# Kernel optimization log

Measured on AMD Instinct MI355X. Metric: run time of the kernel, lower is better.

The kernel has to match this reference:

```python
import jax, jax.numpy as jnp
import numpy as np

B, C_IN, T, H, W = 8, 8, 12, 128, 128
HID = 32
K = 3


def _conv2d(x, w, b):
    # x: (B, Cin, H, W), w: (Cout, Cin, K, K) -> SAME padding, stride 1
    y = jax.lax.conv_general_dilated(
        x, w, window_strides=(1, 1), padding='SAME',
        dimension_numbers=('NCHW', 'OIHW', 'NCHW'))
    return y + b[None, :, None, None]


def setup_inputs() -> dict:
    key = jax.random.key(0)
    k1, k2, k3, k4, k5 = jax.random.split(key, 5)
    x = jax.random.normal(k1, (B, C_IN, T, H, W), dtype=jnp.float32)
    cin = C_IN + HID
    scale = 1.0 / np.sqrt(cin * K * K)
    W_gates = jax.random.normal(k2, (2 * HID, cin, K, K), dtype=jnp.float32) * scale
    b_gates = jax.random.normal(k3, (2 * HID,), dtype=jnp.float32) * 0.01
    W_can = jax.random.normal(k4, (HID, cin, K, K), dtype=jnp.float32) * scale
    b_can = jax.random.normal(k5, (HID,), dtype=jnp.float32) * 0.01
    return {"x": x, "W_gates": W_gates, "b_gates": b_gates,
            "W_can": W_can, "b_can": b_can}


def reference(x, W_gates, b_gates, W_can, b_can):
    # x: (B, C, T, H, W) -> swap to time-major for the recurrence
    xs = jnp.transpose(x, (2, 0, 1, 3, 4))  # (T, B, C, H, W)
    h0 = jnp.zeros((x.shape[0], HID, x.shape[3], x.shape[4]), dtype=x.dtype)

    def step(h, x_t):
        comb = jnp.concatenate([x_t, h], axis=1)          # (B, C+HID, H, W)
        gates = jax.nn.sigmoid(_conv2d(comb, W_gates, b_gates))
        reset, update = jnp.split(gates, 2, axis=1)       # each (B, HID, H, W)
        comb2 = jnp.concatenate([x_t, reset * h], axis=1)
        cand = jnp.tanh(_conv2d(comb2, W_can, b_can))
        h_next = (1.0 - update) * h + update * cand
        return h_next, h_next

    h_last, ys = jax.lax.scan(step, h0, xs)               # ys: (T, B, HID, H, W)
    out = jnp.transpose(ys, (1, 2, 0, 3, 4))              # (B, HID, T, H, W) — swap back
    return out, h_last
```

## Files before the change

### kernel.cpp

```cpp
#include <hip/hip_runtime.h>
#include <hip/hip_bf16.h>
#include <hip/hip_fp16.h>
#include <cmath>

#define BB   8
#define CIN  8
#define TT   12
#define HH   128
#define WW   128
#define HID  32
#define CCOMB 40
#define HW   (HH * WW)
#define NBLK 512

#define S1    44
#define T1W   20
#define OFF2  17600
#define S2    36
#define OFFU  29264
#define SMEM_U16 38480

typedef __attribute__((ext_vector_type(8))) short sv8;
typedef __attribute__((ext_vector_type(4))) short sv4;
typedef __attribute__((ext_vector_type(4))) float f32x4;
typedef unsigned short u16;
typedef unsigned long long ull;

__device__ inline u16 f2bf(float f) {
    union { float f; unsigned u; } v; v.f = f;
    unsigned u = v.u;
    return (u16)((u + 0x7FFFu + ((u >> 16) & 1u)) >> 16);
}
__device__ inline float bf2f(u16 h) {
    union { unsigned u; float f; } v; v.u = ((unsigned)h) << 16; return v.f;
}
__device__ inline float sigmoid_fast(float x) { return 1.f / (1.f + __expf(-x)); }
__device__ inline float tanh_fast(float z) {
    float a = fabsf(z);
    float r = 1.f - 2.f / (__expf(2.f * a) + 1.f);
    return copysignf(r, z);
}

__device__ __forceinline__ void band_rc(int i, int& r, int& c) {
    if (i < 40)      { r = i / 20;            c = i % 20; }
    else if (i < 80) { int j = i - 40; r = 18 + j / 20; c = j % 20; }
    else             { int j = i - 80; r = 2 + (j >> 2);
                       int k = j & 3;  c = (k < 2) ? k : 16 + k; }
}

__device__ inline sv8 gather_wfrag(const float* __restrict__ W,
                                   int co, int g, int kx, int ks) {
    int k0 = ks * 32 + g * 8;
    sv8 f;
    if (k0 < 120) {
        int ky  = k0 / 40;
        int ci0 = k0 - ky * 40;
#pragma unroll
        for (int i = 0; i < 8; ++i)
            f[i] = (short)f2bf(W[(((size_t)co * CCOMB + ci0 + i) * 3 + ky) * 3 + kx]);
    } else {
#pragma unroll
        for (int i = 0; i < 8; ++i) f[i] = 0;
    }
    return f;
}

__global__ void pack_weights(const float* __restrict__ Wg,
                             const float* __restrict__ Wc,
                             u16* __restrict__ pack) {
    int tid = blockIdx.x * blockDim.x + threadIdx.x;
    if (tid >= 6 * 12 * 64) return;
    int lane = tid & 63;
    int f    = (tid >> 6) % 12;
    int Gall = tid / (12 * 64);
    int kx = f >> 2, ks = f & 3;
    int g = lane >> 4;
    sv8 v;
    if (Gall < 4) v = gather_wfrag(Wg, Gall * 16 + (lane & 15), g, kx, ks);
    else          v = gather_wfrag(Wc, (Gall - 4) * 16 + (lane & 15), g, kx, ks);
    *(sv8*)&pack[(size_t)tid * 8] = v;
}

__global__ __launch_bounds__(256) void x_to_bf16(const float* __restrict__ x,
                                                 u16* __restrict__ xbf) {
    int gid = blockIdx.x * 256 + threadIdx.x;
    if (gid >= BB * TT * HW) return;
    int p  = gid & (HW - 1);
    int bt = gid >> 14;
    int t = bt % TT, b = bt / TT;
    sv8 v;
#pragma unroll
    for (int c = 0; c < 8; ++c)
        v[c] = (short)f2bf(x[(((size_t)b * CIN + c) * TT + t) * HW + p]);
    *(sv8*)&xbf[(size_t)gid * 8] = v;
}

#define MFMA16(A, B, C) __builtin_amdgcn_mfma_f32_16x16x32_bf16(A, B, C, 0, 0, 0)

#define GATES_TILE(YY, XX, LVAL, UVALQ)                                        \
    {                                                                          \
        int pb = ((YY) * T1W + (XX)) * S1;                                     \
        f32x4 aA = {0.f,0.f,0.f,0.f}, aB = {0.f,0.f,0.f,0.f};                  \
        _Pragma("unroll")                                                      \
        for (int kx = 0; kx < 3; ++kx)                                         \
        _Pragma("unroll")                                                      \
        for (int ks = 0; ks < 4; ++ks) {                                       \
            int a = pb + kx * S1 + koff1[ks];                                  \
            sv4 lo = *(const sv4*)&smem[a];                                    \
            sv4 hi = *(const sv4*)&smem[a + 4];                                \
            sv8 bv = __builtin_shufflevector(lo, hi, 0,1,2,3,4,5,6,7);         \
            aA = MFMA16(wfA[kx*4+ks], bv, aA);                                 \
            aB = MFMA16(wfB[kx*4+ks], bv, aB);                                 \
        }                                                                      \
        if (coPair == 0) {                                                     \
            int ctr = pb + 21 * S1 + 8;                                        \
            sv4 h4A = *(const sv4*)&smem[ctr + co0A];                          \
            sv4 h4B = *(const sv4*)&smem[ctr + co0B];                          \
            sv4 rhA, rhB;                                                      \
            _Pragma("unroll")                                                  \
            for (int r = 0; r < 4; ++r) {                                      \
                rhA[r] = (short)f2bf(sigmoid_fast(aA[r] + bgA[r]) * bf2f((u16)h4A[r])); \
                rhB[r] = (short)f2bf(sigmoid_fast(aB[r] + bgB[r]) * bf2f((u16)h4B[r])); \
            }                                                                  \
            if (LVAL) {                                                        \
                int o2 = OFF2 + ((YY) * 18 + (XX)) * S2;                       \
                *(sv4*)&smem[o2 + co0A] = rhA;                                 \
                *(sv4*)&smem[o2 + co0B] = rhB;                                 \
            }                                                                  \
        } else {                                                               \
            sv4 uA, uB;                                                        \
            _Pragma("unroll")                                                  \
            for (int r = 0; r < 4; ++r) {                                      \
                uA[r] = (short)__half_as_ushort(__float2half(sigmoid_fast(aA[r] + bgA[r]))); \
                uB[r] = (short)__half_as_ushort(__float2half(sigmoid_fast(aB[r] + bgB[r]))); \
            }                                                                  \
            if ((LVAL) && (UVALQ)) {                                           \
                int uo = OFFU + (((YY) - 1) * 16 + ((XX) - 1)) * S2;           \
                *(sv4*)&smem[uo + (co0A - 32)] = uA;                           \
                *(sv4*)&smem[uo + (co0B - 32)] = uB;                           \
            }                                                                  \
        }                                                                      \
    }

__global__ __launch_bounds__(256)
__attribute__((amdgpu_waves_per_eu(2, 2)))
void gru_persist(
    const u16* __restrict__ xbf, const u16* __restrict__ wpack,
    const float* __restrict__ bg, const float* __restrict__ bc,
    u16* __restrict__ hG, int* __restrict__ flags,
    float* __restrict__ out, float* __restrict__ hlast)
{
    __shared__ __align__(16) u16 smem[SMEM_U16];
    const int id = blockIdx.x;
    const int b = id & 7, tau = id >> 3;
    const int bx = tau & 7, by = tau >> 3;
    const int x0 = bx * 16, y0 = by * 16;
    const int tid = threadIdx.x, lane = tid & 63, w = tid >> 6;
    const int m = lane & 15, g = lane >> 4;

    int nbr = -1;
    if (tid < 8) {
        const int dxs[8] = {-1, 0, 1, -1, 1, -1, 0, 1};
        const int dys[8] = {-1, -1, -1, 0, 0, 1, 1, 1};
        int nx = bx + dxs[tid], ny = by + dys[tid];
        if ((unsigned)nx < 8u && (unsigned)ny < 8u)
            nbr = ((ny * 8 + nx) * 8 + b);
    }

    int koff1[4], coffC[4], kstrC[4];
    bool isX[4];
#pragma unroll
    for (int ks = 0; ks < 4; ++ks) {
        int k0 = ks * 32 + g * 8;
        int ky = 0, ci0 = 0;
        if (k0 < 120) { ky = k0 / 40; ci0 = k0 - ky * 40; }
        koff1[ks] = ky * (T1W * S1) + ci0;
        isX[ks]   = (ci0 == 0);
        coffC[ks] = isX[ks] ? ky * (T1W * S1) : ky * (18 * S2) + (ci0 - 8);
        kstrC[ks] = isX[ks] ? S1 : S2;
    }

    const int coPair = w >> 1;
    const int parity = w & 1;
    const int co0A = coPair * 32 + g * 4;
    const int co0B = co0A + 16;
    const int grpA = coPair * 2, grpB = grpA + 1;

    const int j0 = w * 4;
    int rowb1[4], rowb2[4];
#pragma unroll
    for (int jr = 0; jr < 4; ++jr) {
        rowb1[jr] = ((j0 + jr + 1) * T1W + m + 1) * S1;
        rowb2[jr] = OFF2 + ((j0 + jr) * 18 + m) * S2;
    }

    f32x4 bgA = *(const f32x4*)&bg[co0A];
    f32x4 bgB = *(const f32x4*)&bg[co0B];
    f32x4 bcA = *(const f32x4*)&bc[g * 4];
    f32x4 bcB = *(const f32x4*)&bc[16 + g * 4];
    const int cA = g * 4, cB = 16 + g * 4;

    for (int i = tid; i < 3200; i += 256) {
        int px = i >> 3, q = i & 7;
        *(ull*)&smem[px * S1 + 8 + q * 4] = 0ull;
    }

    const u16* xbB = xbf + (size_t)b * TT * HW * 8;
    const size_t planeElems = (size_t)BB * HW * 32;

    for (int t = 0; t < TT; ++t) {
        const u16* hGr = hG + (size_t)(t & 1) * planeElems + (size_t)b * HW * 32;
        u16*       hGw = hG + (size_t)((t + 1) & 1) * planeElems + (size_t)b * HW * 32;

        sv8 wfA[12], wfB[12];
#pragma unroll
        for (int f = 0; f < 12; ++f) {
            wfA[f] = *(const sv8*)&wpack[(((size_t)grpA * 12 + f) * 64 + lane) * 8];
            wfB[f] = *(const sv8*)&wpack[(((size_t)grpB * 12 + f) * 64 + lane) * 8];
        }

        const u16* xb = xbB + (size_t)t * HW * 8;
        for (int idx = tid; idx < 400; idx += 256) {
            int r = idx / 20, c = idx - r * 20;
            int gy = y0 + r - 2, gx = x0 + c - 2;
            sv8 v = {};
            if ((unsigned)gy < 128u && (unsigned)gx < 128u)
                v = *(const sv8*)&xb[(size_t)(gy * WW + gx) * 8];
            *(sv4*)&smem[idx * S1]     = __builtin_shufflevector(v, v, 0,1,2,3);
            *(sv4*)&smem[idx * S1 + 4] = __builtin_shufflevector(v, v, 4,5,6,7);
        }
        __syncthreads();

        for (int nt = parity; nt < 13; nt += 2) {
            int i = nt * 16 + m;
            bool lval = (i < 196);
            if (i > 195) i = 195;
            int q14 = i / 14;
            int yy = 2 + q14, xx = 2 + (i - q14 * 14);
            GATES_TILE(yy, xx, lval, true);
        }

        if (t > 0) {
            if (tid < 8 && nbr >= 0) {
                while (__hip_atomic_load(&flags[nbr * 32], __ATOMIC_RELAXED,
                                         __HIP_MEMORY_SCOPE_AGENT) < t)
                    __builtin_amdgcn_s_sleep(2);
            }
        }
        __syncthreads();

        for (int idx = tid; idx < 1152; idx += 256) {
            int i = idx >> 3, q = idx & 7;
            int r, c; band_rc(i, r, c);
            int gy = y0 + r - 2, gx = x0 + c - 2;
            ull v = 0;
            if ((unsigned)gy < 128u && (unsigned)gx < 128u)
                v = __hip_atomic_load((const ull*)&hGr[(size_t)(gy * WW + gx) * 32 + q * 4],
                                      __ATOMIC_RELAXED, __HIP_MEMORY_SCOPE_AGENT);
            *(ull*)&smem[(r * T1W + c) * S1 + 8 + q * 4] = v;
        }
        __syncthreads();

        for (int nt = parity; nt < 8; nt += 2) {
            int e = nt * 16 + m;
            int yy, xx;
            if (e < 36)       { int q = e / 18;        yy = q;       xx = e - q * 18; }
            else if (e < 72)  { int j = e - 36; int q = j / 18; yy = 16 + q; xx = j - q * 18; }
            else if (e < 100) { int j = e - 72;  yy = 2 + (j >> 1); xx = (j & 1); }
            else              { int j = e - 100; yy = 2 + (j >> 1); xx = 16 + (j & 1); }
            bool uval = (yy >= 1 && yy <= 16 && xx >= 1 && xx <= 16);
            GATES_TILE(yy, xx, true, uval);
        }

        sv8 wcA[12], wcB[12];
#pragma unroll
        for (int f = 0; f < 12; ++f) {
            wcA[f] = *(const sv8*)&wpack[(((size_t)4 * 12 + f) * 64 + lane) * 8];
            wcB[f] = *(const sv8*)&wpack[(((size_t)5 * 12 + f) * 64 + lane) * 8];
        }
        __syncthreads();

        f32x4 a2A[4], a2B[4];
#pragma unroll
        for (int jr = 0; jr < 4; ++jr) {
            a2A[jr] = (f32x4){0.f,0.f,0.f,0.f};
            a2B[jr] = (f32x4){0.f,0.f,0.f,0.f};
        }
#pragma unroll
        for (int kx = 0; kx < 3; ++kx)
#pragma unroll
            for (int ks = 0; ks < 4; ++ks) {
#pragma unroll
                for (int jr = 0; jr < 4; ++jr) {
                    int a = (isX[ks] ? rowb1[jr] : rowb2[jr]) + coffC[ks] + kx * kstrC[ks];
                    sv4 lo = *(const sv4*)&smem[a];
                    sv4 hi = *(const sv4*)&smem[a + 4];
                    sv8 bv = __builtin_shufflevector(lo, hi, 0,1,2,3,4,5,6,7);
                    a2A[jr] = MFMA16(wcA[kx*4+ks], bv, a2A[jr]);
                    a2B[jr] = MFMA16(wcB[kx*4+ks], bv, a2B[jr]);
                }
            }

#pragma unroll
        for (int jr = 0; jr < 4; ++jr) {
            int j = j0 + jr;
            int gy = y0 + j, gx = x0 + m;
            int ctr = ((j + 2) * T1W + m + 2) * S1 + 8;
            int ub  = OFFU + (j * 16 + m) * S2;
            sv4 h4A = *(const sv4*)&smem[ctr + cA];
            sv4 h4B = *(const sv4*)&smem[ctr + cB];
            sv4 u4A = *(const sv4*)&smem[ub + cA];
            sv4 u4B = *(const sv4*)&smem[ub + cB];
            sv4 hnA, hnB;
#pragma unroll
            for (int r = 0; r < 4; ++r) {
                float cv = tanh_fast(a2A[jr][r] + bcA[r]);
                float uu = __half2float(__ushort_as_half((u16)u4A[r]));
                float hn = (1.f - uu) * bf2f((u16)h4A[r]) + uu * cv;
                a2A[jr][r] = hn; hnA[r] = (short)f2bf(hn);
                cv = tanh_fast(a2B[jr][r] + bcB[r]);
                uu = __half2float(__ushort_as_half((u16)u4B[r]));
                hn = (1.f - uu) * bf2f((u16)h4B[r]) + uu * cv;
                a2B[jr][r] = hn; hnB[r] = (short)f2bf(hn);
            }
            *(sv4*)&smem[ctr + cA] = hnA;
            *(sv4*)&smem[ctr + cB] = hnB;
            if (j <= 1 || j >= 14 || m <= 1 || m >= 14) {
                union { sv4 s; ull u; } ca, cb; ca.s = hnA; cb.s = hnB;
                ull* base = (ull*)&hGw[(size_t)(gy * WW + gx) * 32];
                __hip_atomic_store(base + (cA >> 2), ca.u, __ATOMIC_RELAXED,
                                   __HIP_MEMORY_SCOPE_AGENT);
                __hip_atomic_store(base + (cB >> 2), cb.u, __ATOMIC_RELAXED,
                                   __HIP_MEMORY_SCOPE_AGENT);
            }
        }

        asm volatile("s_waitcnt vmcnt(0)" ::: "memory");
        __syncthreads();
        if (tid == 0)
            __hip_atomic_store(&flags[id * 32], t + 1, __ATOMIC_RELAXED,
                               __HIP_MEMORY_SCOPE_AGENT);

#pragma unroll
        for (int jr = 0; jr < 4; ++jr) {
            int j = j0 + jr;
            int gy = y0 + j, gx = x0 + m;
#pragma unroll
            for (int r = 0; r < 4; ++r) {
                __builtin_nontemporal_store(a2A[jr][r],
                    &out[(((size_t)b * HID + cA + r) * TT + t) * HW + (size_t)gy * WW + gx]);
                __builtin_nontemporal_store(a2B[jr][r],
                    &out[(((size_t)b * HID + cB + r) * TT + t) * HW + (size_t)gy * WW + gx]);
                if (t == TT - 1) {
                    __builtin_nontemporal_store(a2A[jr][r],
                        &hlast[((size_t)b * HID + cA + r) * HW + (size_t)gy * WW + gx]);
                    __builtin_nontemporal_store(a2B[jr][r],
                        &hlast[((size_t)b * HID + cB + r) * HW + (size_t)gy * WW + gx]);
                }
            }
        }
    }
}

extern "C" void kernel_launch(void* const* d_in, const int* in_sizes, int n_in,
                              void* d_out, int out_size, void* d_ws, size_t ws_size,
                              hipStream_t stream) {
    const float* x  = (const float*)d_in[0];
    const float* Wg = (const float*)d_in[1];
    const float* bg = (const float*)d_in[2];
    const float* Wc = (const float*)d_in[3];
    const float* bc = (const float*)d_in[4];

    float* out   = (float*)d_out;
    float* hlast = out + (size_t)BB * HID * TT * HW;

    const size_t PLANEB = (size_t)BB * HW * 32 * sizeof(u16);
    const size_t PACKB  = (size_t)6 * 12 * 64 * 8 * sizeof(u16);
    const size_t FLAGB  = (size_t)NBLK * 32 * sizeof(int);
    char* ws = (char*)d_ws;
    u16* hG    = (u16*)ws;
    u16* wpack = (u16*)(ws + 2 * PLANEB);
    int* flags = (int*)(ws + 2 * PLANEB + PACKB);
    u16* xbf   = (u16*)(ws + 2 * PLANEB + PACKB + FLAGB);

    pack_weights<<<(6 * 12 * 64 + 255) / 256, 256, 0, stream>>>(Wg, Wc, wpack);
    x_to_bf16<<<(BB * TT * HW) / 256, 256, 0, stream>>>(x, xbf);
    hipMemsetAsync(hG, 0, PLANEB, stream);
    hipMemsetAsync(flags, 0, FLAGB, stream);

    gru_persist<<<NBLK, 256, 0, stream>>>(xbf, wpack, bg, bc, hG, flags,
                                          out, hlast);
}
```

Measured before the change: 471.7 us.

## Exchange halo through per-block compact outbox with 16-byte coherent loads/stores

Replaces the full-size global hidden-state planes with a compact per-block outbox holding only the 144 border pixels each block's neighbours need. The halo is now written from LDS after a barrier as 16-byte coherent stores and read as 16-byte loads with precomputed offsets, instead of 8-byte atomic accesses scattered across the image. Candidate-weight loading is moved earlier so it overlaps the halo fetch. The change adds an extra barrier and inline asm with sc0/sc1 cache bits, and relies on the outbox mapping being correct for neighbours at tile edges.

Measured after the change: 561.5 us. 1.19x slower.

```diff
diff --git a/kernel.cpp b/kernel.cpp
--- a/kernel.cpp
+++ b/kernel.cpp
@@ -20,9 +20,13 @@
 #define OFFU  29264
 #define SMEM_U16 38480
 
+#define OB_BLK   4608
+#define OB_PLANE ((size_t)NBLK * OB_BLK)
+
 typedef __attribute__((ext_vector_type(8))) short sv8;
 typedef __attribute__((ext_vector_type(4))) short sv4;
 typedef __attribute__((ext_vector_type(4))) float f32x4;
+typedef __attribute__((ext_vector_type(4))) unsigned u32x4;
 typedef unsigned short u16;
 typedef unsigned long long ull;
 
@@ -47,6 +51,29 @@
     else             { int j = i - 80; r = 2 + (j >> 2);
                        int k = j & 3;  c = (k < 2) ? k : 16 + k; }
 }
+
+__device__ __forceinline__ void obox_rc(int px, int& r, int& c) {
+    if (px < 32)       { r = px >> 4;               c = px & 15; }
+    else if (px < 64)  { int i = px - 32;  r = 14 + (i >> 4); c = i & 15; }
+    else if (px < 96)  { int i = px - 64;  r = i >> 1;        c = i & 1; }
+    else if (px < 128) { int i = px - 96;  r = i >> 1;        c = 14 + (i & 1); }
+    else if (px < 132) { int i = px - 128; r = i >> 1;        c = i & 1; }
+    else if (px < 136) { int i = px - 132; r = i >> 1;        c = 14 + (i & 1); }
+    else if (px < 140) { int i = px - 136; r = 14 + (i >> 1); c = i & 1; }
+    else               { int i = px - 140; r = 14 + (i >> 1); c = 14 + (i & 1); }
+}
+
+__device__ __forceinline__ u32x4 coh_load16(const u16* p) {
+    u32x4 v;
+    asm volatile("global_load_dwordx4 %0, %1, off sc0 sc1"
+                 : "=v"(v) : "v"(p) : "memory");
+    return v;
+}
+__device__ __forceinline__ void coh_store16(u16* p, u32x4 v) {
+    asm volatile("global_store_dwordx4 %0, %1, off sc0 sc1"
+                 :: "v"(p), "v"(v) : "memory");
+}
+#define VMCNT0 asm volatile("s_waitcnt vmcnt(0)" ::: "memory")
 
 __device__ inline sv8 gather_wfrag(const float* __restrict__ W,
                                    int co, int g, int kx, int ks) {
@@ -147,7 +174,7 @@
 void gru_persist(
     const u16* __restrict__ xbf, const u16* __restrict__ wpack,
     const float* __restrict__ bg, const float* __restrict__ bc,
-    u16* __restrict__ hG, int* __restrict__ flags,
+    u16* __restrict__ obox, int* __restrict__ flags,
     float* __restrict__ out, float* __restrict__ hlast)
 {
     __shared__ __align__(16) u16 smem[SMEM_U16];
@@ -200,17 +227,52 @@
     f32x4 bcB = *(const f32x4*)&bc[16 + g * 4];
     const int cA = g * 4, cB = 16 + g * 4;
 
+    int cLds[3], cOff[3]; bool cVal[3];
+    int pLds[3], pOff[3]; bool pVal[3];
+#pragma unroll
+    for (int k = 0; k < 3; ++k) {
+        int u = tid + k * 256;
+        cVal[k] = false; pVal[k] = false;
+        cLds[k] = 0; cOff[k] = 0; pLds[k] = 0; pOff[k] = 0;
+        if (u < 576) {
+            int px = u >> 2, q = u & 3;
+            int r, c; band_rc(px, r, c);
+            int dy = (r < 2) ? -1 : (r >= 18 ? 1 : 0);
+            int dx = (c < 2) ? -1 : (c >= 18 ? 1 : 0);
+            int ny = by + dy, nx = bx + dx;
+            if ((unsigned)ny < 8u && (unsigned)nx < 8u) {
+                int rn = r - 2 - dy * 16, cn = c - 2 - dx * 16;
+                int base, spx;
+                if (dy == -1 && dx == 0)      { base = 32;  spx = (rn - 14) * 16 + cn; }
+                else if (dy == 1 && dx == 0)  { base = 0;   spx = rn * 16 + cn; }
+                else if (dy == 0 && dx == -1) { base = 96;  spx = rn * 2 + (cn - 14); }
+                else if (dy == 0 && dx == 1)  { base = 64;  spx = rn * 2 + cn; }
+                else if (dy == -1 && dx == -1){ base = 140; spx = (rn - 14) * 2 + (cn - 14); }
+                else if (dy == -1 && dx == 1) { base = 136; spx = (rn - 14) * 2 + cn; }
+                else if (dy == 1 && dx == -1) { base = 132; spx = rn * 2 + (cn - 14); }
+                else                          { base = 128; spx = rn * 2 + cn; }
+                int nbid = (ny * 8 + nx) * 8 + b;
+                cVal[k] = true;
+                cLds[k] = (r * T1W + c) * S1 + 8 + q * 8;
+                cOff[k] = nbid * OB_BLK + (base + spx) * 32 + q * 8;
+            }
+            int pr, pc; obox_rc(px, pr, pc);
+            pVal[k] = true;
+            pLds[k] = ((pr + 2) * T1W + (pc + 2)) * S1 + 8 + q * 8;
+            pOff[k] = id * OB_BLK + px * 32 + q * 8;
+        }
+    }
+
     for (int i = tid; i < 3200; i += 256) {
         int px = i >> 3, q = i & 7;
         *(ull*)&smem[px * S1 + 8 + q * 4] = 0ull;
     }
 
     const u16* xbB = xbf + (size_t)b * TT * HW * 8;
-    const size_t planeElems = (size_t)BB * HW * 32;
 
     for (int t = 0; t < TT; ++t) {
-        const u16* hGr = hG + (size_t)(t & 1) * planeElems + (size_t)b * HW * 32;
-        u16*       hGw = hG + (size_t)((t + 1) & 1) * planeElems + (size_t)b * HW * 32;
+        const u16* ob_r = obox + (size_t)(t & 1) * OB_PLANE;
+        u16*       ob_w = obox + (size_t)((t + 1) & 1) * OB_PLANE;
 
         sv8 wfA[12], wfB[12];
 #pragma unroll
@@ -249,15 +311,31 @@
         }
         __syncthreads();
 
-        for (int idx = tid; idx < 1152; idx += 256) {
-            int i = idx >> 3, q = idx & 7;
-            int r, c; band_rc(i, r, c);
-            int gy = y0 + r - 2, gx = x0 + c - 2;
-            ull v = 0;
-            if ((unsigned)gy < 128u && (unsigned)gx < 128u)
-                v = __hip_atomic_load((const ull*)&hGr[(size_t)(gy * WW + gx) * 32 + q * 4],
-                                      __ATOMIC_RELAXED, __HIP_MEMORY_SCOPE_AGENT);
-            *(ull*)&smem[(r * T1W + c) * S1 + 8 + q * 4] = v;
+        {
+            u32x4 v0 = {}, v1 = {}, v2 = {};
+            if (cVal[0]) v0 = coh_load16(ob_r + cOff[0]);
+            if (cVal[1]) v1 = coh_load16(ob_r + cOff[1]);
+            if (cVal[2]) v2 = coh_load16(ob_r + cOff[2]);
+            VMCNT0;
+            if (cVal[0]) {
+                *(ull*)&smem[cLds[0]]     = ((ull)v0.y << 32) | v0.x;
+                *(ull*)&smem[cLds[0] + 4] = ((ull)v0.w << 32) | v0.z;
+            }
+            if (cVal[1]) {
+                *(ull*)&smem[cLds[1]]     = ((ull)v1.y << 32) | v1.x;
+                *(ull*)&smem[cLds[1] + 4] = ((ull)v1.w << 32) | v1.z;
+            }
+            if (cVal[2]) {
+                *(ull*)&smem[cLds[2]]     = ((ull)v2.y << 32) | v2.x;
+                *(ull*)&smem[cLds[2] + 4] = ((ull)v2.w << 32) | v2.z;
+            }
+        }
+
+        sv8 wcA[12], wcB[12];
+#pragma unroll
+        for (int f = 0; f < 12; ++f) {
+            wcA[f] = *(const sv8*)&wpack[(((size_t)4 * 12 + f) * 64 + lane) * 8];
+            wcB[f] = *(const sv8*)&wpack[(((size_t)5 * 12 + f) * 64 + lane) * 8];
         }
         __syncthreads();
 
@@ -271,13 +349,6 @@
             bool uval = (yy >= 1 && yy <= 16 && xx >= 1 && xx <= 16);
             GATES_TILE(yy, xx, true, uval);
         }
-
-        sv8 wcA[12], wcB[12];
-#pragma unroll
-        for (int f = 0; f < 12; ++f) {
-            wcA[f] = *(const sv8*)&wpack[(((size_t)4 * 12 + f) * 64 + lane) * 8];
-            wcB[f] = *(const sv8*)&wpack[(((size_t)5 * 12 + f) * 64 + lane) * 8];
-        }
         __syncthreads();
 
         f32x4 a2A[4], a2B[4];
@@ -304,7 +375,6 @@
 #pragma unroll
         for (int jr = 0; jr < 4; ++jr) {
             int j = j0 + jr;
-            int gy = y0 + j, gx = x0 + m;
             int ctr = ((j + 2) * T1W + m + 2) * S1 + 8;
             int ub  = OFFU + (j * 16 + m) * S2;
             sv4 h4A = *(const sv4*)&smem[ctr + cA];
@@ -325,37 +395,54 @@
             }
             *(sv4*)&smem[ctr + cA] = hnA;
             *(sv4*)&smem[ctr + cB] = hnB;
-            if (j <= 1 || j >= 14 || m <= 1 || m >= 14) {
-                union { sv4 s; ull u; } ca, cb; ca.s = hnA; cb.s = hnB;
-                ull* base = (ull*)&hGw[(size_t)(gy * WW + gx) * 32];
-                __hip_atomic_store(base + (cA >> 2), ca.u, __ATOMIC_RELAXED,
-                                   __HIP_MEMORY_SCOPE_AGENT);
-                __hip_atomic_store(base + (cB >> 2), cb.u, __ATOMIC_RELAXED,
-                                   __HIP_MEMORY_SCOPE_AGENT);
-            }
-        }
-
-        asm volatile("s_waitcnt vmcnt(0)" ::: "memory");
+        }
+        __syncthreads();
+
+        {
+            if (pVal[0]) {
+                ull lo = *(const ull*)&smem[pLds[0]];
+                ull hi = *(const ull*)&smem[pLds[0] + 4];
+                u32x4 v = { (unsigned)lo, (unsigned)(lo >> 32),
+                            (unsigned)hi, (unsigned)(hi >> 32) };
+                coh_store16(ob_w + pOff[0], v);
+            }
+            if (pVal[1]) {
+                ull lo = *(const ull*)&smem[pLds[1]];
+                ull hi = *(const ull*)&smem[pLds[1] + 4];
+                u32x4 v = { (unsigned)lo, (unsigned)(lo >> 32),
+                            (unsigned)hi, (unsigned)(hi >> 32) };
+                coh_store16(ob_w + pOff[1], v);
+            }
+            if (pVal[2]) {
+                ull lo = *(const ull*)&smem[pLds[2]];
+                ull hi = *(const ull*)&smem[pLds[2] + 4];
+                u32x4 v = { (unsigned)lo, (unsigned)(lo >> 32),
+                            (unsigned)hi, (unsigned)(hi >> 32) };
+                coh_store16(ob_w + pOff[2], v);
+            }
+        }
+        VMCNT0;
         __syncthreads();
         if (tid == 0)
             __hip_atomic_store(&flags[id * 32], t + 1, __ATOMIC_RELAXED,
                                __HIP_MEMORY_SCOPE_AGENT);
 
+        int gxo = x0 + m;
 #pragma unroll
         for (int jr = 0; jr < 4; ++jr) {
             int j = j0 + jr;
-            int gy = y0 + j, gx = x0 + m;
+            int gy = y0 + j;
 #pragma unroll
             for (int r = 0; r < 4; ++r) {
                 __builtin_nontemporal_store(a2A[jr][r],
-                    &out[(((size_t)b * HID + cA + r) * TT + t) * HW + (size_t)gy * WW + gx]);
+                    &out[(((size_t)b * HID + cA + r) * TT + t) * HW + (size_t)gy * WW + gxo]);
                 __builtin_nontemporal_store(a2B[jr][r],
-                    &out[(((size_t)b * HID + cB + r) * TT + t) * HW + (size_t)gy * WW + gx]);
+                    &out[(((size_t)b * HID + cB + r) * TT + t) * HW + (size_t)gy * WW + gxo]);
                 if (t == TT - 1) {
                     __builtin_nontemporal_store(a2A[jr][r],
-                        &hlast[((size_t)b * HID + cA + r) * HW + (size_t)gy * WW + gx]);
+                        &hlast[((size_t)b * HID + cA + r) * HW + (size_t)gy * WW + gxo]);
                     __builtin_nontemporal_store(a2B[jr][r],
-                        &hlast[((size_t)b * HID + cB + r) * HW + (size_t)gy * WW + gx]);
+                        &hlast[((size_t)b * HID + cB + r) * HW + (size_t)gy * WW + gxo]);
                 }
             }
         }
@@ -374,20 +461,20 @@
     float* out   = (float*)d_out;
     float* hlast = out + (size_t)BB * HID * TT * HW;
 
-    const size_t PLANEB = (size_t)BB * HW * 32 * sizeof(u16);
-    const size_t PACKB  = (size_t)6 * 12 * 64 * 8 * sizeof(u16);
-    const size_t FLAGB  = (size_t)NBLK * 32 * sizeof(int);
+    const size_t OBOXB = 2 * OB_PLANE * sizeof(u16);
+    const size_t PACKB = (size_t)6 * 12 * 64 * 8 * sizeof(u16);
+    const size_t FLAGB = (size_t)NBLK * 32 * sizeof(int);
     char* ws = (char*)d_ws;
-    u16* hG    = (u16*)ws;
-    u16* wpack = (u16*)(ws + 2 * PLANEB);
-    int* flags = (int*)(ws + 2 * PLANEB + PACKB);
-    u16* xbf   = (u16*)(ws + 2 * PLANEB + PACKB + FLAGB);
+    u16* obox  = (u16*)ws;
+    u16* wpack = (u16*)(ws + OBOXB);
+    int* flags = (int*)(ws + OBOXB + PACKB);
+    u16* xbf   = (u16*)(ws + OBOXB + PACKB + FLAGB);
 
     pack_weights<<<(6 * 12 * 64 + 255) / 256, 256, 0, stream>>>(Wg, Wc, wpack);
     x_to_bf16<<<(BB * TT * HW) / 256, 256, 0, stream>>>(x, xbf);
-    hipMemsetAsync(hG, 0, PLANEB, stream);
+    hipMemsetAsync(obox, 0, OB_PLANE * sizeof(u16), stream);
     hipMemsetAsync(flags, 0, FLAGB, stream);
 
-    gru_persist<<<NBLK, 256, 0, stream>>>(xbf, wpack, bg, bc, hG, flags,
+    gru_persist<<<NBLK, 256, 0, stream>>>(xbf, wpack, bg, bc, obox, flags,
                                           out, hlast);
 }
```

## Double block threads to 512 and split output channels across more waves

Applied to the files above, without the earlier changes.

Launches the persistent GRU kernel with 512 threads (8 waves) instead of 256. Each wave now handles one 16-channel output group instead of a pair, which halves the weight fragments and accumulators held per wave. The intent is more wave-level parallelism and latency hiding inside each block during the MFMA convolution phases, with the same grid of 512 persistent blocks. The cost is heavier __syncthreads barriers and a stricter per-wave register budget (waves_per_eu 4), which could cause spilling or reduce how many blocks fit per CU.

Result: slower. 593.2 us (+25.7%).

```diff
diff --git a/kernel.cpp b/kernel.cpp
--- a/kernel.cpp
+++ b/kernel.cpp
@@ -97,10 +97,10 @@
 
 #define MFMA16(A, B, C) __builtin_amdgcn_mfma_f32_16x16x32_bf16(A, B, C, 0, 0, 0)
 
-#define GATES_TILE(YY, XX, LVAL, UVALQ)                                        \
+#define GATES_TILE1(YY, XX, LVAL, UVALQ)                                       \
     {                                                                          \
         int pb = ((YY) * T1W + (XX)) * S1;                                     \
-        f32x4 aA = {0.f,0.f,0.f,0.f}, aB = {0.f,0.f,0.f,0.f};                  \
+        f32x4 aa = {0.f,0.f,0.f,0.f};                                          \
         _Pragma("unroll")                                                      \
         for (int kx = 0; kx < 3; ++kx)                                         \
         _Pragma("unroll")                                                      \
@@ -109,41 +109,31 @@
             sv4 lo = *(const sv4*)&smem[a];                                    \
             sv4 hi = *(const sv4*)&smem[a + 4];                                \
             sv8 bv = __builtin_shufflevector(lo, hi, 0,1,2,3,4,5,6,7);         \
-            aA = MFMA16(wfA[kx*4+ks], bv, aA);                                 \
-            aB = MFMA16(wfB[kx*4+ks], bv, aB);                                 \
+            aa = MFMA16(wf[kx*4+ks], bv, aa);                                  \
         }                                                                      \
-        if (coPair == 0) {                                                     \
+        if (gw < 2) {                                                          \
             int ctr = pb + 21 * S1 + 8;                                        \
-            sv4 h4A = *(const sv4*)&smem[ctr + co0A];                          \
-            sv4 h4B = *(const sv4*)&smem[ctr + co0B];                          \
-            sv4 rhA, rhB;                                                      \
+            sv4 h4 = *(const sv4*)&smem[ctr + co0g];                           \
+            sv4 rh4;                                                           \
             _Pragma("unroll")                                                  \
-            for (int r = 0; r < 4; ++r) {                                      \
-                rhA[r] = (short)f2bf(sigmoid_fast(aA[r] + bgA[r]) * bf2f((u16)h4A[r])); \
-                rhB[r] = (short)f2bf(sigmoid_fast(aB[r] + bgB[r]) * bf2f((u16)h4B[r])); \
-            }                                                                  \
+            for (int r = 0; r < 4; ++r)                                        \
+                rh4[r] = (short)f2bf(sigmoid_fast(aa[r] + bga[r]) * bf2f((u16)h4[r])); \
             if (LVAL) {                                                        \
-                int o2 = OFF2 + ((YY) * 18 + (XX)) * S2;                       \
-                *(sv4*)&smem[o2 + co0A] = rhA;                                 \
-                *(sv4*)&smem[o2 + co0B] = rhB;                                 \
+                *(sv4*)&smem[OFF2 + ((YY) * 18 + (XX)) * S2 + co0g] = rh4;     \
             }                                                                  \
         } else {                                                               \
-            sv4 uA, uB;                                                        \
+            sv4 uv;                                                            \
             _Pragma("unroll")                                                  \
-            for (int r = 0; r < 4; ++r) {                                      \
-                uA[r] = (short)__half_as_ushort(__float2half(sigmoid_fast(aA[r] + bgA[r]))); \
-                uB[r] = (short)__half_as_ushort(__float2half(sigmoid_fast(aB[r] + bgB[r]))); \
-            }                                                                  \
+            for (int r = 0; r < 4; ++r)                                        \
+                uv[r] = (short)__half_as_ushort(__float2half(sigmoid_fast(aa[r] + bga[r]))); \
             if ((LVAL) && (UVALQ)) {                                           \
-                int uo = OFFU + (((YY) - 1) * 16 + ((XX) - 1)) * S2;           \
-                *(sv4*)&smem[uo + (co0A - 32)] = uA;                           \
-                *(sv4*)&smem[uo + (co0B - 32)] = uB;                           \
+                *(sv4*)&smem[OFFU + (((YY) - 1) * 16 + ((XX) - 1)) * S2 + (co0g - 32)] = uv; \
             }                                                                  \
         }                                                                      \
     }
 
-__global__ __launch_bounds__(256)
-__attribute__((amdgpu_waves_per_eu(2, 2)))
+__global__ __launch_bounds__(512)
+__attribute__((amdgpu_waves_per_eu(4, 4)))
 void gru_persist(
     const u16* __restrict__ xbf, const u16* __restrict__ wpack,
     const float* __restrict__ bg, const float* __restrict__ bc,
@@ -180,27 +170,22 @@
         kstrC[ks] = isX[ks] ? S1 : S2;
     }
 
-    const int coPair = w >> 1;
-    const int parity = w & 1;
-    const int co0A = coPair * 32 + g * 4;
-    const int co0B = co0A + 16;
-    const int grpA = coPair * 2, grpB = grpA + 1;
-
-    const int j0 = w * 4;
+    const int gw = w & 3, ph = w >> 2;
+    const int co0g = gw * 16 + g * 4;
+    const int cg = w & 1, rp = w >> 1;
+    const int co0c = cg * 16 + g * 4;
+
     int rowb1[4], rowb2[4];
 #pragma unroll
     for (int jr = 0; jr < 4; ++jr) {
-        rowb1[jr] = ((j0 + jr + 1) * T1W + m + 1) * S1;
-        rowb2[jr] = OFF2 + ((j0 + jr) * 18 + m) * S2;
-    }
-
-    f32x4 bgA = *(const f32x4*)&bg[co0A];
-    f32x4 bgB = *(const f32x4*)&bg[co0B];
-    f32x4 bcA = *(const f32x4*)&bc[g * 4];
-    f32x4 bcB = *(const f32x4*)&bc[16 + g * 4];
-    const int cA = g * 4, cB = 16 + g * 4;
-
-    for (int i = tid; i < 3200; i += 256) {
+        rowb1[jr] = ((rp * 4 + jr + 1) * T1W + m + 1) * S1;
+        rowb2[jr] = OFF2 + ((rp * 4 + jr) * 18 + m) * S2;
+    }
+
+    f32x4 bga = *(const f32x4*)&bg[co0g];
+    f32x4 bca = *(const f32x4*)&bc[co0c];
+
+    for (int i = tid; i < 3200; i += 512) {
         int px = i >> 3, q = i & 7;
         *(ull*)&smem[px * S1 + 8 + q * 4] = 0ull;
     }
@@ -212,32 +197,30 @@
         const u16* hGr = hG + (size_t)(t & 1) * planeElems + (size_t)b * HW * 32;
         u16*       hGw = hG + (size_t)((t + 1) & 1) * planeElems + (size_t)b * HW * 32;
 
-        sv8 wfA[12], wfB[12];
-#pragma unroll
-        for (int f = 0; f < 12; ++f) {
-            wfA[f] = *(const sv8*)&wpack[(((size_t)grpA * 12 + f) * 64 + lane) * 8];
-            wfB[f] = *(const sv8*)&wpack[(((size_t)grpB * 12 + f) * 64 + lane) * 8];
-        }
+        sv8 wf[12];
+#pragma unroll
+        for (int f = 0; f < 12; ++f)
+            wf[f] = *(const sv8*)&wpack[(((size_t)gw * 12 + f) * 64 + lane) * 8];
 
         const u16* xb = xbB + (size_t)t * HW * 8;
-        for (int idx = tid; idx < 400; idx += 256) {
-            int r = idx / 20, c = idx - r * 20;
+        if (tid < 400) {
+            int r = tid / 20, c = tid - r * 20;
             int gy = y0 + r - 2, gx = x0 + c - 2;
             sv8 v = {};
             if ((unsigned)gy < 128u && (unsigned)gx < 128u)
                 v = *(const sv8*)&xb[(size_t)(gy * WW + gx) * 8];
-            *(sv4*)&smem[idx * S1]     = __builtin_shufflevector(v, v, 0,1,2,3);
-            *(sv4*)&smem[idx * S1 + 4] = __builtin_shufflevector(v, v, 4,5,6,7);
-        }
-        __syncthreads();
-
-        for (int nt = parity; nt < 13; nt += 2) {
+            *(sv4*)&smem[tid * S1]     = __builtin_shufflevector(v, v, 0,1,2,3);
+            *(sv4*)&smem[tid * S1 + 4] = __builtin_shufflevector(v, v, 4,5,6,7);
+        }
+        __syncthreads();
+
+        for (int nt = ph; nt < 13; nt += 2) {
             int i = nt * 16 + m;
             bool lval = (i < 196);
             if (i > 195) i = 195;
             int q14 = i / 14;
             int yy = 2 + q14, xx = 2 + (i - q14 * 14);
-            GATES_TILE(yy, xx, lval, true);
+            GATES_TILE1(yy, xx, lval, true);
         }
 
         if (t > 0) {
@@ -249,7 +232,7 @@
         }
         __syncthreads();
 
-        for (int idx = tid; idx < 1152; idx += 256) {
+        for (int idx = tid; idx < 1152; idx += 512) {
             int i = idx >> 3, q = idx & 7;
             int r, c; band_rc(i, r, c);
             int gy = y0 + r - 2, gx = x0 + c - 2;
@@ -261,7 +244,7 @@
         }
         __syncthreads();
 
-        for (int nt = parity; nt < 8; nt += 2) {
+        for (int nt = ph; nt < 8; nt += 2) {
             int e = nt * 16 + m;
             int yy, xx;
             if (e < 36)       { int q = e / 18;        yy = q;       xx = e - q * 18; }
@@ -269,23 +252,18 @@
             else if (e < 100) { int j = e - 72;  yy = 2 + (j >> 1); xx = (j & 1); }
             else              { int j = e - 100; yy = 2 + (j >> 1); xx = 16 + (j & 1); }
             bool uval = (yy >= 1 && yy <= 16 && xx >= 1 && xx <= 16);
-            GATES_TILE(yy, xx, true, uval);
-        }
-
-        sv8 wcA[12], wcB[12];
-#pragma unroll
-        for (int f = 0; f < 12; ++f) {
-            wcA[f] = *(const sv8*)&wpack[(((size_t)4 * 12 + f) * 64 + lane) * 8];
-            wcB[f] = *(const sv8*)&wpack[(((size_t)5 * 12 + f) * 64 + lane) * 8];
-        }
-        __syncthreads();
-
-        f32x4 a2A[4], a2B[4];
-#pragma unroll
-        for (int jr = 0; jr < 4; ++jr) {
-            a2A[jr] = (f32x4){0.f,0.f,0.f,0.f};
-            a2B[jr] = (f32x4){0.f,0.f,0.f,0.f};
-        }
+            GATES_TILE1(yy, xx, true, uval);
+        }
+
+        sv8 wc[12];
+#pragma unroll
+        for (int f = 0; f < 12; ++f)
+            wc[f] = *(const sv8*)&wpack[(((size_t)(4 + cg) * 12 + f) * 64 + lane) * 8];
+        __syncthreads();
+
+        f32x4 a2[4];
+#pragma unroll
+        for (int jr = 0; jr < 4; ++jr) a2[jr] = (f32x4){0.f,0.f,0.f,0.f};
 #pragma unroll
         for (int kx = 0; kx < 3; ++kx)
 #pragma unroll
@@ -296,42 +274,31 @@
                     sv4 lo = *(const sv4*)&smem[a];
                     sv4 hi = *(const sv4*)&smem[a + 4];
                     sv8 bv = __builtin_shufflevector(lo, hi, 0,1,2,3,4,5,6,7);
-                    a2A[jr] = MFMA16(wcA[kx*4+ks], bv, a2A[jr]);
-                    a2B[jr] = MFMA16(wcB[kx*4+ks], bv, a2B[jr]);
+                    a2[jr] = MFMA16(wc[kx*4+ks], bv, a2[jr]);
                 }
             }
 
 #pragma unroll
         for (int jr = 0; jr < 4; ++jr) {
-            int j = j0 + jr;
+            int j = rp * 4 + jr;
             int gy = y0 + j, gx = x0 + m;
             int ctr = ((j + 2) * T1W + m + 2) * S1 + 8;
             int ub  = OFFU + (j * 16 + m) * S2;
-            sv4 h4A = *(const sv4*)&smem[ctr + cA];
-            sv4 h4B = *(const sv4*)&smem[ctr + cB];
-            sv4 u4A = *(const sv4*)&smem[ub + cA];
-            sv4 u4B = *(const sv4*)&smem[ub + cB];
-            sv4 hnA, hnB;
+            sv4 h4 = *(const sv4*)&smem[ctr + co0c];
+            sv4 u4 = *(const sv4*)&smem[ub + co0c];
+            sv4 hn4;
 #pragma unroll
             for (int r = 0; r < 4; ++r) {
-                float cv = tanh_fast(a2A[jr][r] + bcA[r]);
-                float uu = __half2float(__ushort_as_half((u16)u4A[r]));
-                float hn = (1.f - uu) * bf2f((u16)h4A[r]) + uu * cv;
-                a2A[jr][r] = hn; hnA[r] = (short)f2bf(hn);
-                cv = tanh_fast(a2B[jr][r] + bcB[r]);
-                uu = __half2float(__ushort_as_half((u16)u4B[r]));
-                hn = (1.f - uu) * bf2f((u16)h4B[r]) + uu * cv;
-                a2B[jr][r] = hn; hnB[r] = (short)f2bf(hn);
-            }
-            *(sv4*)&smem[ctr + cA] = hnA;
-            *(sv4*)&smem[ctr + cB] = hnB;
+                float cv = tanh_fast(a2[jr][r] + bca[r]);
+                float uu = __half2float(__ushort_as_half((u16)u4[r]));
+                float hn = (1.f - uu) * bf2f((u16)h4[r]) + uu * cv;
+                a2[jr][r] = hn; hn4[r] = (short)f2bf(hn);
+            }
+            *(sv4*)&smem[ctr + co0c] = hn4;
             if (j <= 1 || j >= 14 || m <= 1 || m >= 14) {
-                union { sv4 s; ull u; } ca, cb; ca.s = hnA; cb.s = hnB;
-                ull* base = (ull*)&hGw[(size_t)(gy * WW + gx) * 32];
-                __hip_atomic_store(base + (cA >> 2), ca.u, __ATOMIC_RELAXED,
-                                   __HIP_MEMORY_SCOPE_AGENT);
-                __hip_atomic_store(base + (cB >> 2), cb.u, __ATOMIC_RELAXED,
-                                   __HIP_MEMORY_SCOPE_AGENT);
+                union { sv4 s; ull u; } cvt; cvt.s = hn4;
+                __hip_atomic_store((ull*)&hGw[(size_t)(gy * WW + gx) * 32 + co0c],
+                                   cvt.u, __ATOMIC_RELAXED, __HIP_MEMORY_SCOPE_AGENT);
             }
         }
 
@@ -343,20 +310,15 @@
 
 #pragma unroll
         for (int jr = 0; jr < 4; ++jr) {
-            int j = j0 + jr;
+            int j = rp * 4 + jr;
             int gy = y0 + j, gx = x0 + m;
 #pragma unroll
             for (int r = 0; r < 4; ++r) {
-                __builtin_nontemporal_store(a2A[jr][r],
-                    &out[(((size_t)b * HID + cA + r) * TT + t) * HW + (size_t)gy * WW + gx]);
-                __builtin_nontemporal_store(a2B[jr][r],
-                    &out[(((size_t)b * HID + cB + r) * TT + t) * HW + (size_t)gy * WW + gx]);
-                if (t == TT - 1) {
-                    __builtin_nontemporal_store(a2A[jr][r],
-                        &hlast[((size_t)b * HID + cA + r) * HW + (size_t)gy * WW + gx]);
-                    __builtin_nontemporal_store(a2B[jr][r],
-                        &hlast[((size_t)b * HID + cB + r) * HW + (size_t)gy * WW + gx]);
-                }
+                __builtin_nontemporal_store(a2[jr][r],
+                    &out[(((size_t)b * HID + co0c + r) * TT + t) * HW + (size_t)gy * WW + gx]);
+                if (t == TT - 1)
+                    __builtin_nontemporal_store(a2[jr][r],
+                        &hlast[((size_t)b * HID + co0c + r) * HW + (size_t)gy * WW + gx]);
             }
         }
     }
@@ -388,6 +350,6 @@
     hipMemsetAsync(hG, 0, PLANEB, stream);
     hipMemsetAsync(flags, 0, FLAGB, stream);
 
-    gru_persist<<<NBLK, 256, 0, stream>>>(xbf, wpack, bg, bc, hG, flags,
+    gru_persist<<<NBLK, 512, 0, stream>>>(xbf, wpack, bg, bc, hG, flags,
                                           out, hlast);
 }
```

## Merge interior and halo gate passes after neighbor wait; pad LDS strides

Applied to the files above, without the earlier changes.

Drops the split where the interior gate tiles were computed before waiting on neighbor flags and the halo band after. All 18x18 gate pixels are now computed in one pass once the neighbor h is loaded, which removes a barrier and the irregular halo indexing. LDS strides S1 and S2 are padded (44->46, 36->38) to reduce bank conflicts, while the update buffer keeps a stride of 36. The cost is that interior gate work no longer overlaps the spin-wait on neighbors, which may lengthen the critical path of the recurrence. Launch bounds are also changed from waves_per_eu(2,2) to __launch_bounds__(256,2).

Measured after the change: 475.7 us. Within noise of the previous version (+0.8%).

```diff
diff --git a/kernel.cpp b/kernel.cpp
--- a/kernel.cpp
+++ b/kernel.cpp
@@ -13,12 +13,12 @@
 #define HW   (HH * WW)
 #define NBLK 512
 
-#define S1    44
+#define S1    46
 #define T1W   20
-#define OFF2  17600
-#define S2    36
-#define OFFU  29264
-#define SMEM_U16 38480
+#define OFF2  18400
+#define S2    38
+#define OFFU  30712
+#define SMEM_U16 39928
 
 typedef __attribute__((ext_vector_type(8))) short sv8;
 typedef __attribute__((ext_vector_type(4))) short sv4;
@@ -135,16 +135,14 @@
                 uB[r] = (short)__half_as_ushort(__float2half(sigmoid_fast(aB[r] + bgB[r]))); \
             }                                                                  \
             if ((LVAL) && (UVALQ)) {                                           \
-                int uo = OFFU + (((YY) - 1) * 16 + ((XX) - 1)) * S2;           \
-                *(sv4*)&smem[uo + (co0A - 32)] = uA;                           \
-                *(sv4*)&smem[uo + (co0B - 32)] = uB;                           \
+                int ub = OFFU + (((YY) - 1) * 16 + ((XX) - 1)) * 36;           \
+                *(sv4*)&smem[ub + (co0A - 32)] = uA;                           \
+                *(sv4*)&smem[ub + (co0B - 32)] = uB;                           \
             }                                                                  \
         }                                                                      \
     }
 
-__global__ __launch_bounds__(256)
-__attribute__((amdgpu_waves_per_eu(2, 2)))
-void gru_persist(
+__global__ __launch_bounds__(256, 2) void gru_persist(
     const u16* __restrict__ xbf, const u16* __restrict__ wpack,
     const float* __restrict__ bg, const float* __restrict__ bc,
     u16* __restrict__ hG, int* __restrict__ flags,
@@ -229,16 +227,6 @@
             *(sv4*)&smem[idx * S1]     = __builtin_shufflevector(v, v, 0,1,2,3);
             *(sv4*)&smem[idx * S1 + 4] = __builtin_shufflevector(v, v, 4,5,6,7);
         }
-        __syncthreads();
-
-        for (int nt = parity; nt < 13; nt += 2) {
-            int i = nt * 16 + m;
-            bool lval = (i < 196);
-            if (i > 195) i = 195;
-            int q14 = i / 14;
-            int yy = 2 + q14, xx = 2 + (i - q14 * 14);
-            GATES_TILE(yy, xx, lval, true);
-        }
 
         if (t > 0) {
             if (tid < 8 && nbr >= 0) {
@@ -246,8 +234,8 @@
                                          __HIP_MEMORY_SCOPE_AGENT) < t)
                     __builtin_amdgcn_s_sleep(2);
             }
-        }
-        __syncthreads();
+            __syncthreads();
+        }
 
         for (int idx = tid; idx < 1152; idx += 256) {
             int i = idx >> 3, q = idx & 7;
@@ -261,15 +249,13 @@
         }
         __syncthreads();
 
-        for (int nt = parity; nt < 8; nt += 2) {
-            int e = nt * 16 + m;
-            int yy, xx;
-            if (e < 36)       { int q = e / 18;        yy = q;       xx = e - q * 18; }
-            else if (e < 72)  { int j = e - 36; int q = j / 18; yy = 16 + q; xx = j - q * 18; }
-            else if (e < 100) { int j = e - 72;  yy = 2 + (j >> 1); xx = (j & 1); }
-            else              { int j = e - 100; yy = 2 + (j >> 1); xx = 16 + (j & 1); }
+        for (int nt = parity; nt < 21; nt += 2) {
+            int px = nt * 16 + m;
+            bool val = px < 324;
+            if (!val) px = 323;
+            int yy = px / 18, xx = px - yy * 18;
             bool uval = (yy >= 1 && yy <= 16 && xx >= 1 && xx <= 16);
-            GATES_TILE(yy, xx, true, uval);
+            GATES_TILE(yy, xx, val, uval);
         }
 
         sv8 wcA[12], wcB[12];
@@ -306,7 +292,7 @@
             int j = j0 + jr;
             int gy = y0 + j, gx = x0 + m;
             int ctr = ((j + 2) * T1W + m + 2) * S1 + 8;
-            int ub  = OFFU + (j * 16 + m) * S2;
+            int ub  = OFFU + (j * 16 + m) * 36;
             sv4 h4A = *(const sv4*)&smem[ctr + cA];
             sv4 h4B = *(const sv4*)&smem[ctr + cB];
             sv4 u4A = *(const sv4*)&smem[ub + cA];
@@ -385,8 +371,8 @@
 
     pack_weights<<<(6 * 12 * 64 + 255) / 256, 256, 0, stream>>>(Wg, Wc, wpack);
     x_to_bf16<<<(BB * TT * HW) / 256, 256, 0, stream>>>(x, xbf);
-    hipMemsetAsync(hG, 0, PLANEB, stream);
-    hipMemsetAsync(flags, 0, FLAGB, stream);
+    (void)hipMemsetAsync(hG, 0, PLANEB, stream);
+    (void)hipMemsetAsync(flags, 0, FLAGB, stream);
 
     gru_persist<<<NBLK, 256, 0, stream>>>(xbf, wpack, bg, bc, hG, flags,
                                           out, hlast);
```
